# Kernel optimization log

Measured on AMD Instinct MI355X. Metric: run time of the kernel, lower is better.

## Reference

```python
import jax, jax.numpy as jnp
import numpy as np

B, S, E = 4, 2048, 512
Q, FFN = 8, 2048


def setup_inputs() -> dict:
    key = jax.random.key(0)
    k_x, k_th, k_w1, k_w2 = jax.random.split(key, 4)
    x = jax.random.normal(k_x, (B, S, E), dtype=jnp.float32)
    # trainable RY angles, one per wire
    theta = jax.random.normal(k_th, (Q,), dtype=jnp.float32)
    W1 = jax.random.normal(k_w1, (Q, FFN), dtype=jnp.float32) / np.sqrt(Q)
    b1 = jnp.zeros((FFN,), dtype=jnp.float32)
    W2 = jax.random.normal(k_w2, (FFN, E), dtype=jnp.float32) / np.sqrt(FFN)
    b2 = jnp.zeros((E,), dtype=jnp.float32)
    return {"x": x, "theta": theta, "W1": W1, "b1": b1, "W2": W2, "b2": b2}


def reference(x, theta, W1, b1, W2, b2):
    # Quantum circuit: |0> -> RX(x_i) -> RY(theta_i) -> <Z> per wire.
    # No entangling gates, so the 8-qubit state factorizes; simulate each
    # qubit's 2 complex amplitudes, batched over all tokens & wires at once.
    n_wires = theta.shape[0]
    xq = x[..., :n_wires]                     # encoder uses input_idx 0..7: [B,S,Q]
    # RX(x)|0> = cos(x/2)|0> - i sin(x/2)|1>
    a = jnp.cos(xq * 0.5).astype(jnp.complex64)
    b = (-1j) * jnp.sin(xq * 0.5).astype(jnp.complex64)
    # RY(theta) = [[c,-s],[s,c]], c=cos(theta/2), s=sin(theta/2)
    c = jnp.cos(theta * 0.5).astype(jnp.complex64)
    s = jnp.sin(theta * 0.5).astype(jnp.complex64)
    a2 = c * a - s * b
    b2_ = s * a + c * b
    # <Z> = |amp0|^2 - |amp1|^2  -> [B,S,Q]
    z = (jnp.abs(a2) ** 2 - jnp.abs(b2_) ** 2).astype(x.dtype)
    # dropout is identity at inference
    h = jax.nn.relu(jnp.einsum('bsq,qf->bsf', z, W1) + b1)
    return jnp.einsum('bsf,fe->bse', h, W2) + b2
```

## Files before the change

### kernel.cpp

```cpp
#include <hip/hip_runtime.h>
#include <hip/hip_bf16.h>

typedef __bf16 bf16_t;
typedef __bf16 bf16x4 __attribute__((ext_vector_type(4)));
typedef __bf16 bf16x8 __attribute__((ext_vector_type(8)));
typedef float f32x4 __attribute__((ext_vector_type(4)));

#define M_TOT 8192
#define N_TOT 512
#define K_TOT 2048
#define E_TOT 512
#define NT    (K_TOT / 64)

typedef const __attribute__((address_space(1))) void* gas_ptr;
typedef __attribute__((address_space(3))) void* las_ptr;

__device__ __forceinline__ void gload_lds16(const void* g, void* l) {
    __builtin_amdgcn_global_load_lds((gas_ptr)g, (las_ptr)l, 16, 0, 0);
}

__device__ __forceinline__ bf16x8 zero8() {
    bf16x8 v;
#pragma unroll
    for (int i = 0; i < 8; ++i) v[i] = (bf16_t)0.0f;
    return v;
}

__global__ __launch_bounds__(256)
void prep3_kernel(const float* __restrict__ x,
                  const float* __restrict__ theta,
                  const float* __restrict__ W1,
                  const float* __restrict__ b1,
                  const float* __restrict__ W2,
                  bf16_t* __restrict__ W2t,
                  bf16_t* __restrict__ zb,
                  bf16_t* __restrict__ W1t)
{
    const int b = blockIdx.x;
    if (b < 256) {
        __shared__ bf16_t T[64][66];
        const int k0 = (b >> 3) * 64;
        const int n0 = (b & 7) * 64;
        const int kl = threadIdx.x >> 4;
        const int n4 = threadIdx.x & 15;
#pragma unroll
        for (int i = 0; i < 4; ++i) {
            int k = kl + i * 16;
            float4 v = *(const float4*)(W2 + (size_t)(k0 + k) * N_TOT + n0 + n4 * 4);
            T[n4 * 4 + 0][k] = (bf16_t)v.x;
            T[n4 * 4 + 1][k] = (bf16_t)v.y;
            T[n4 * 4 + 2][k] = (bf16_t)v.z;
            T[n4 * 4 + 3][k] = (bf16_t)v.w;
        }
        __syncthreads();
        const int nl = threadIdx.x >> 4;
        const int k4 = threadIdx.x & 15;
#pragma unroll
        for (int i = 0; i < 4; ++i) {
            int n = nl + i * 16;
            bf16x4 v;
            v[0] = T[n][k4 * 4 + 0];
            v[1] = T[n][k4 * 4 + 1];
            v[2] = T[n][k4 * 4 + 2];
            v[3] = T[n][k4 * 4 + 3];
            *(bf16x4*)(W2t + (size_t)(n0 + n) * K_TOT + k0 + k4 * 4) = v;
        }
    } else if (b < 288) {
        const int m = (b - 256) * 256 + threadIdx.x;
        float4 x0 = *(const float4*)(x + (size_t)m * E_TOT);
        float4 x1 = *(const float4*)(x + (size_t)m * E_TOT + 4);
        float xs[8] = {x0.x, x0.y, x0.z, x0.w, x1.x, x1.y, x1.z, x1.w};
        bf16x8 lo;
#pragma unroll
        for (int q = 0; q < 8; ++q)
            lo[q] = (bf16_t)(__builtin_cosf(theta[q]) * __builtin_cosf(xs[q]));
        bf16x8 hi = zero8();
        hi[0] = (bf16_t)1.0f;
        *(bf16x8*)(zb + (size_t)m * 16)     = lo;
        *(bf16x8*)(zb + (size_t)m * 16 + 8) = hi;
    } else {
        const int f = (b - 288) * 256 + threadIdx.x;
        bf16x8 lo;
#pragma unroll
        for (int q = 0; q < 8; ++q)
            lo[q] = (bf16_t)W1[(size_t)q * K_TOT + f];
        bf16x8 hi = zero8();
        hi[0] = (bf16_t)b1[f];
        *(bf16x8*)(W1t + (size_t)f * 16)     = lo;
        *(bf16x8*)(W1t + (size_t)f * 16 + 8) = hi;
    }
}

__device__ __forceinline__ void load_wf(const bf16_t* __restrict__ W1t, int k0,
                                        int l15, int lq, bf16x8 wf[4]) {
#pragma unroll
    for (int ft = 0; ft < 4; ++ft) wf[ft] = zero8();
    if (lq < 2) {
#pragma unroll
        for (int ft = 0; ft < 4; ++ft)
            wf[ft] = *(const bf16x8*)(W1t + (size_t)(k0 + ft * 16 + l15) * 16 + lq * 8);
    }
}

__device__ __forceinline__ void stage_B(const bf16_t* __restrict__ W2t, int n_base,
                                        int k0, bf16_t* Bb, int w, int lrow, int lseg) {
#pragma unroll
    for (int j = 0; j < 4; ++j) {
        int n = j * 32 + w * 8 + lrow;
        int g = lseg ^ (n & 7);
        gload_lds16(W2t + (size_t)(n_base + n) * K_TOT + k0 + g * 8,
                    Bb + j * 2048 + w * 512);
    }
}

__device__ __forceinline__ void h_stage(const bf16x8 wf[4], const bf16x8 zfrag[2],
                                        bf16_t* Ab, int w, int l15, int lq) {
#pragma unroll
    for (int mh = 0; mh < 2; ++mh) {
        int m_loc = w * 32 + mh * 16 + l15;
#pragma unroll
        for (int ft = 0; ft < 4; ++ft) {
            f32x4 hacc = (f32x4){0.f, 0.f, 0.f, 0.f};
            hacc = __builtin_amdgcn_mfma_f32_16x16x32_bf16(wf[ft], zfrag[mh], hacc, 0, 0, 0);
            bf16x4 hv;
#pragma unroll
            for (int r = 0; r < 4; ++r) hv[r] = (bf16_t)fmaxf(hacc[r], 0.f);
            int fseg = ft * 2 + (lq >> 1);
            int slot = fseg ^ (m_loc & 7);
            *(bf16x4*)(Ab + m_loc * 64 + slot * 8 + (lq & 1) * 4) = hv;
        }
    }
}

__device__ __forceinline__ void main_mfma(const bf16_t* Ab, const bf16_t* Bb,
                                          int wm, int wn, int l15, int lq,
                                          f32x4 acc[4][4]) {
#pragma unroll
    for (int kk = 0; kk < 2; ++kk) {
        bf16x8 af[4], bfr[4];
#pragma unroll
        for (int mt = 0; mt < 4; ++mt) {
            int r = wm * 64 + mt * 16 + l15;
            int s = (kk * 4 + lq) ^ (r & 7);
            af[mt] = *(const bf16x8*)(Ab + r * 64 + s * 8);
        }
#pragma unroll
        for (int nt = 0; nt < 4; ++nt) {
            int r = wn * 64 + nt * 16 + l15;
            int s = (kk * 4 + lq) ^ (r & 7);
            bfr[nt] = *(const bf16x8*)(Bb + r * 64 + s * 8);
        }
#pragma unroll
        for (int mt = 0; mt < 4; ++mt)
#pragma unroll
            for (int nt = 0; nt < 4; ++nt)
                acc[mt][nt] = __builtin_amdgcn_mfma_f32_16x16x32_bf16(
                    af[mt], bfr[nt], acc[mt][nt], 0, 0, 0);
    }
}

__global__ __launch_bounds__(256)
void ffq_gemm_kernel(const bf16_t* __restrict__ zb,
                     const bf16_t* __restrict__ W1t,
                     const bf16_t* __restrict__ W2t,
                     const float* __restrict__ b2,
                     float* __restrict__ out)
{
    __shared__ bf16_t Alds[2][128 * 64];
    __shared__ bf16_t Blds[2][128 * 64];

    const int t = threadIdx.x;
    const int w = t >> 6, l = t & 63;
    const int m_base = blockIdx.y * 128;
    const int n_base = blockIdx.x * 128;
    const int wm = w >> 1, wn = w & 1;
    const int l15 = l & 15, lq = l >> 4;
    const int lrow = l >> 3, lseg = l & 7;

    bf16x8 zfrag[2];
#pragma unroll
    for (int mh = 0; mh < 2; ++mh) {
        zfrag[mh] = zero8();
        if (lq < 2)
            zfrag[mh] = *(const bf16x8*)(zb + (size_t)(m_base + w * 32 + mh * 16 + l15) * 16 + lq * 8);
    }

    f32x4 acc[4][4];
#pragma unroll
    for (int mt = 0; mt < 4; ++mt)
#pragma unroll
        for (int nt = 0; nt < 4; ++nt)
            acc[mt][nt] = (f32x4){0.f, 0.f, 0.f, 0.f};

    {
        bf16x8 wf0[4];
        load_wf(W1t, 0, l15, lq, wf0);
        stage_B(W2t, n_base, 0, Blds[0], w, lrow, lseg);
        h_stage(wf0, zfrag, Alds[0], w, l15, lq);
    }

    for (int it = 0; it < NT; it += 2) {
        bf16x8 wfa[4];
        load_wf(W1t, (it + 1) * 64, l15, lq, wfa);
        __syncthreads();
        stage_B(W2t, n_base, (it + 1) * 64, Blds[1], w, lrow, lseg);
        h_stage(wfa, zfrag, Alds[1], w, l15, lq);
        main_mfma(Alds[0], Blds[0], wm, wn, l15, lq, acc);

        bf16x8 wfb[4];
        if (it + 2 < NT) load_wf(W1t, (it + 2) * 64, l15, lq, wfb);
        __syncthreads();
        if (it + 2 < NT) {
            stage_B(W2t, n_base, (it + 2) * 64, Blds[0], w, lrow, lseg);
            h_stage(wfb, zfrag, Alds[0], w, l15, lq);
        }
        main_mfma(Alds[1], Blds[1], wm, wn, l15, lq, acc);
    }

#pragma unroll
    for (int nt = 0; nt < 4; ++nt) {
        int col = n_base + wn * 64 + nt * 16 + l15;
        float bias = b2[col];
#pragma unroll
        for (int mt = 0; mt < 4; ++mt) {
#pragma unroll
            for (int r = 0; r < 4; ++r) {
                int row = m_base + wm * 64 + mt * 16 + lq * 4 + r;
                out[(size_t)row * N_TOT + col] = acc[mt][nt][r] + bias;
            }
        }
    }
}

extern "C" void kernel_launch(void* const* d_in, const int* in_sizes, int n_in,
                              void* d_out, int out_size, void* d_ws, size_t ws_size,
                              hipStream_t stream) {
    const float* x     = (const float*)d_in[0];
    const float* theta = (const float*)d_in[1];
    const float* W1    = (const float*)d_in[2];
    const float* b1    = (const float*)d_in[3];
    const float* W2    = (const float*)d_in[4];
    const float* b2    = (const float*)d_in[5];
    float* out = (float*)d_out;

    const size_t W2T_BYTES = (size_t)N_TOT * K_TOT * sizeof(bf16_t);
    const size_t ZB_BYTES  = (size_t)M_TOT * 16 * sizeof(bf16_t);

    bf16_t* W2t = (bf16_t*)d_ws;
    bf16_t* zb  = (bf16_t*)((char*)d_ws + W2T_BYTES);
    bf16_t* W1t = (bf16_t*)((char*)d_ws + W2T_BYTES + ZB_BYTES);

    prep3_kernel<<<296, 256, 0, stream>>>(x, theta, W1, b1, W2, W2t, zb, W1t);

    dim3 grid(N_TOT / 128, M_TOT / 128);
    ffq_gemm_kernel<<<grid, 256, 0, stream>>>(zb, W1t, W2t, b2, out);
}
```

Baseline: 120.3 us.

## Split K across two wave groups with 512-thread blocks and register-staged B loads

Doubles the block to 8 waves. Each pair of wave groups splits the 64-wide K chunk in halves, and their partial accumulators are reduced through LDS at the end. B tiles now go through registers with plain vector loads instead of direct global-to-LDS loads, and the loads are issued ahead of the MFMA work to hide latency. The change aims to raise per-CU wave occupancy and overlap, at the cost of an extra LDS reduction, more register pressure and extra LDS store traffic for B.

```diff
diff --git a/kernel.cpp b/kernel.cpp
--- a/kernel.cpp
+++ b/kernel.cpp
@@ -10,14 +10,7 @@
 #define N_TOT 512
 #define K_TOT 2048
 #define E_TOT 512
-#define NT    (K_TOT / 64)
-
-typedef const __attribute__((address_space(1))) void* gas_ptr;
-typedef __attribute__((address_space(3))) void* las_ptr;
-
-__device__ __forceinline__ void gload_lds16(const void* g, void* l) {
-    __builtin_amdgcn_global_load_lds((gas_ptr)g, (las_ptr)l, 16, 0, 0);
-}
+#define NT    32
 
 __device__ __forceinline__ bf16x8 zero8() {
     bf16x8 v;
@@ -91,6 +84,26 @@
     }
 }
 
+__device__ __forceinline__ void load_B(const bf16_t* __restrict__ W2t, int n_base,
+                                       int k0, int t, uint4 gv[2]) {
+#pragma unroll
+    for (int j = 0; j < 2; ++j) {
+        int s = t + j * 512;
+        int n = s >> 3;
+        int g = (s & 7) ^ (n & 7);
+        gv[j] = *(const uint4*)(W2t + (size_t)(n_base + n) * K_TOT + k0 + g * 8);
+    }
+}
+__device__ __forceinline__ void write_B(bf16_t* Bb, int t, const uint4 gv[2]) {
+#pragma unroll
+    for (int j = 0; j < 2; ++j) {
+        int s = t + j * 512;
+        int n = s >> 3;
+        int seg = s & 7;
+        *(uint4*)(Bb + n * 64 + seg * 8) = gv[j];
+    }
+}
+
 __device__ __forceinline__ void load_wf(const bf16_t* __restrict__ W1t, int k0,
                                         int l15, int lq, bf16x8 wf[4]) {
 #pragma unroll
@@ -102,64 +115,48 @@
     }
 }
 
-__device__ __forceinline__ void stage_B(const bf16_t* __restrict__ W2t, int n_base,
-                                        int k0, bf16_t* Bb, int w, int lrow, int lseg) {
-#pragma unroll
-    for (int j = 0; j < 4; ++j) {
-        int n = j * 32 + w * 8 + lrow;
-        int g = lseg ^ (n & 7);
-        gload_lds16(W2t + (size_t)(n_base + n) * K_TOT + k0 + g * 8,
-                    Bb + j * 2048 + w * 512);
-    }
-}
-
-__device__ __forceinline__ void h_stage(const bf16x8 wf[4], const bf16x8 zfrag[2],
+__device__ __forceinline__ void h_stage(const bf16x8 wf[4], const bf16x8 zfrag,
                                         bf16_t* Ab, int w, int l15, int lq) {
-#pragma unroll
-    for (int mh = 0; mh < 2; ++mh) {
-        int m_loc = w * 32 + mh * 16 + l15;
-#pragma unroll
-        for (int ft = 0; ft < 4; ++ft) {
-            f32x4 hacc = (f32x4){0.f, 0.f, 0.f, 0.f};
-            hacc = __builtin_amdgcn_mfma_f32_16x16x32_bf16(wf[ft], zfrag[mh], hacc, 0, 0, 0);
-            bf16x4 hv;
-#pragma unroll
-            for (int r = 0; r < 4; ++r) hv[r] = (bf16_t)fmaxf(hacc[r], 0.f);
-            int fseg = ft * 2 + (lq >> 1);
-            int slot = fseg ^ (m_loc & 7);
-            *(bf16x4*)(Ab + m_loc * 64 + slot * 8 + (lq & 1) * 4) = hv;
-        }
+    const int m_loc = w * 16 + l15;
+#pragma unroll
+    for (int ft = 0; ft < 4; ++ft) {
+        f32x4 hacc = (f32x4){0.f, 0.f, 0.f, 0.f};
+        hacc = __builtin_amdgcn_mfma_f32_16x16x32_bf16(wf[ft], zfrag, hacc, 0, 0, 0);
+        bf16x4 hv;
+#pragma unroll
+        for (int r = 0; r < 4; ++r) hv[r] = (bf16_t)fmaxf(hacc[r], 0.f);
+        int fseg = ft * 2 + (lq >> 1);
+        int slot = fseg ^ (m_loc & 7);
+        *(bf16x4*)(Ab + m_loc * 64 + slot * 8 + (lq & 1) * 4) = hv;
     }
 }
 
 __device__ __forceinline__ void main_mfma(const bf16_t* Ab, const bf16_t* Bb,
-                                          int wm, int wn, int l15, int lq,
+                                          int wk, int wm, int wn, int l15, int lq,
                                           f32x4 acc[4][4]) {
-#pragma unroll
-    for (int kk = 0; kk < 2; ++kk) {
-        bf16x8 af[4], bfr[4];
-#pragma unroll
-        for (int mt = 0; mt < 4; ++mt) {
-            int r = wm * 64 + mt * 16 + l15;
-            int s = (kk * 4 + lq) ^ (r & 7);
-            af[mt] = *(const bf16x8*)(Ab + r * 64 + s * 8);
-        }
-#pragma unroll
-        for (int nt = 0; nt < 4; ++nt) {
-            int r = wn * 64 + nt * 16 + l15;
-            int s = (kk * 4 + lq) ^ (r & 7);
-            bfr[nt] = *(const bf16x8*)(Bb + r * 64 + s * 8);
-        }
-#pragma unroll
-        for (int mt = 0; mt < 4; ++mt)
-#pragma unroll
-            for (int nt = 0; nt < 4; ++nt)
-                acc[mt][nt] = __builtin_amdgcn_mfma_f32_16x16x32_bf16(
-                    af[mt], bfr[nt], acc[mt][nt], 0, 0, 0);
-    }
-}
-
-__global__ __launch_bounds__(256)
+    bf16x8 af[4], bfr[4];
+    const int c = wk * 4 + lq;
+#pragma unroll
+    for (int mt = 0; mt < 4; ++mt) {
+        int r = wm * 64 + mt * 16 + l15;
+        int s = c ^ (r & 7);
+        af[mt] = *(const bf16x8*)(Ab + r * 64 + s * 8);
+    }
+#pragma unroll
+    for (int nt = 0; nt < 4; ++nt) {
+        int r = wn * 64 + nt * 16 + l15;
+        int s = c ^ (r & 7);
+        bfr[nt] = *(const bf16x8*)(Bb + r * 64 + s * 8);
+    }
+#pragma unroll
+    for (int mt = 0; mt < 4; ++mt)
+#pragma unroll
+        for (int nt = 0; nt < 4; ++nt)
+            acc[mt][nt] = __builtin_amdgcn_mfma_f32_16x16x32_bf16(
+                af[mt], bfr[nt], acc[mt][nt], 0, 0, 0);
+}
+
+__global__ __launch_bounds__(512, 2)
 void ffq_gemm_kernel(const bf16_t* __restrict__ zb,
                      const bf16_t* __restrict__ W1t,
                      const bf16_t* __restrict__ W2t,
@@ -173,17 +170,12 @@
     const int w = t >> 6, l = t & 63;
     const int m_base = blockIdx.y * 128;
     const int n_base = blockIdx.x * 128;
-    const int wm = w >> 1, wn = w & 1;
+    const int wk = w >> 2, wm = (w >> 1) & 1, wn = w & 1;
     const int l15 = l & 15, lq = l >> 4;
-    const int lrow = l >> 3, lseg = l & 7;
-
-    bf16x8 zfrag[2];
-#pragma unroll
-    for (int mh = 0; mh < 2; ++mh) {
-        zfrag[mh] = zero8();
-        if (lq < 2)
-            zfrag[mh] = *(const bf16x8*)(zb + (size_t)(m_base + w * 32 + mh * 16 + l15) * 16 + lq * 8);
-    }
+
+    bf16x8 zfrag = zero8();
+    if (lq < 2)
+        zfrag = *(const bf16x8*)(zb + (size_t)(m_base + w * 16 + l15) * 16 + lq * 8);
 
     f32x4 acc[4][4];
 #pragma unroll
@@ -192,41 +184,64 @@
         for (int nt = 0; nt < 4; ++nt)
             acc[mt][nt] = (f32x4){0.f, 0.f, 0.f, 0.f};
 
-    {
-        bf16x8 wf0[4];
-        load_wf(W1t, 0, l15, lq, wf0);
-        stage_B(W2t, n_base, 0, Blds[0], w, lrow, lseg);
-        h_stage(wf0, zfrag, Alds[0], w, l15, lq);
-    }
+    uint4 gv[2];
+    bf16x8 wfA[4], wfB[4];
+
+    load_B(W2t, n_base, 0, t, gv);
+    load_wf(W1t, 0, l15, lq, wfA);
+    write_B(Blds[0], t, gv);
+    h_stage(wfA, zfrag, Alds[0], w, l15, lq);
+    load_wf(W1t, 64, l15, lq, wfB);
 
     for (int it = 0; it < NT; it += 2) {
-        bf16x8 wfa[4];
-        load_wf(W1t, (it + 1) * 64, l15, lq, wfa);
         __syncthreads();
-        stage_B(W2t, n_base, (it + 1) * 64, Blds[1], w, lrow, lseg);
-        h_stage(wfa, zfrag, Alds[1], w, l15, lq);
-        main_mfma(Alds[0], Blds[0], wm, wn, l15, lq, acc);
-
-        bf16x8 wfb[4];
-        if (it + 2 < NT) load_wf(W1t, (it + 2) * 64, l15, lq, wfb);
+        load_B(W2t, n_base, (it + 1) * 64, t, gv);
+        if (it + 2 < NT) load_wf(W1t, (it + 2) * 64, l15, lq, wfA);
+        h_stage(wfB, zfrag, Alds[1], w, l15, lq);
+        main_mfma(Alds[0], Blds[0], wk, wm, wn, l15, lq, acc);
+        write_B(Blds[1], t, gv);
+
         __syncthreads();
         if (it + 2 < NT) {
-            stage_B(W2t, n_base, (it + 2) * 64, Blds[0], w, lrow, lseg);
-            h_stage(wfb, zfrag, Alds[0], w, l15, lq);
-        }
-        main_mfma(Alds[1], Blds[1], wm, wn, l15, lq, acc);
-    }
-
-#pragma unroll
-    for (int nt = 0; nt < 4; ++nt) {
-        int col = n_base + wn * 64 + nt * 16 + l15;
-        float bias = b2[col];
-#pragma unroll
-        for (int mt = 0; mt < 4; ++mt) {
-#pragma unroll
-            for (int r = 0; r < 4; ++r) {
-                int row = m_base + wm * 64 + mt * 16 + lq * 4 + r;
-                out[(size_t)row * N_TOT + col] = acc[mt][nt][r] + bias;
+            load_B(W2t, n_base, (it + 2) * 64, t, gv);
+            if (it + 3 < NT) load_wf(W1t, (it + 3) * 64, l15, lq, wfB);
+            h_stage(wfA, zfrag, Alds[0], w, l15, lq);
+        }
+        main_mfma(Alds[1], Blds[1], wk, wm, wn, l15, lq, acc);
+        if (it + 2 < NT) write_B(Blds[0], t, gv);
+    }
+
+    __syncthreads();
+    float* red;
+    {
+        int reg = wm * 2 + wn;
+        red = (reg < 2) ? ((float*)&Alds[0][0] + reg * 4096)
+                        : ((float*)&Blds[0][0] + (reg - 2) * 4096);
+    }
+    if (wk == 1) {
+#pragma unroll
+        for (int mt = 0; mt < 4; ++mt)
+#pragma unroll
+            for (int nt = 0; nt < 4; ++nt)
+#pragma unroll
+                for (int r = 0; r < 4; ++r)
+                    red[(mt * 16 + lq * 4 + r) * 64 + nt * 16 + l15] = acc[mt][nt][r];
+    }
+    __syncthreads();
+    if (wk == 0) {
+#pragma unroll
+        for (int nt = 0; nt < 4; ++nt) {
+            int col = n_base + wn * 64 + nt * 16 + l15;
+            float bias = b2[col];
+#pragma unroll
+            for (int mt = 0; mt < 4; ++mt) {
+#pragma unroll
+                for (int r = 0; r < 4; ++r) {
+                    int row = m_base + wm * 64 + mt * 16 + lq * 4 + r;
+                    float v = acc[mt][nt][r] + bias +
+                              red[(mt * 16 + lq * 4 + r) * 64 + nt * 16 + l15];
+                    out[(size_t)row * N_TOT + col] = v;
+                }
             }
         }
     }
@@ -253,5 +268,5 @@
     prep3_kernel<<<296, 256, 0, stream>>>(x, theta, W1, b1, W2, W2t, zb, W1t);
 
     dim3 grid(N_TOT / 128, M_TOT / 128);
-    ffq_gemm_kernel<<<grid, 256, 0, stream>>>(zb, W1t, W2t, b2, out);
-}
+    ffq_gemm_kernel<<<grid, 512, 0, stream>>>(zb, W1t, W2t, b2, out);
+}
```

After: 121.2 us. No clear change (+0.7%).
